# Kernel tuning notes

Measured on AMD Instinct MI355X. Metric: run time of the kernel, lower is better.

Reference implementation:

```python
import jax, jax.numpy as jnp
import numpy as np

NUM_USERS = 50000
NUM_ITEMS = 100000
N = NUM_USERS + NUM_ITEMS
D = 64
K = 3
E = 1000000


def setup_inputs() -> dict:
    key = jax.random.key(0)
    k1, k2, k3, k4 = jax.random.split(key, 4)
    users_emb = jax.random.normal(k1, (NUM_USERS, D), dtype=jnp.float32)
    items_emb = jax.random.normal(k2, (NUM_ITEMS, D), dtype=jnp.float32)
    src = jax.random.randint(k3, (E,), 0, N, dtype=jnp.int32)
    dst = jax.random.randint(k4, (E,), 0, N, dtype=jnp.int32)
    return {"users_emb": users_emb, "items_emb": items_emb, "src": src, "dst": dst}


def reference(users_emb, items_emb, src, dst):
    all_emb = jnp.concatenate([users_emb, items_emb], axis=0)  # [N, D]
    # out_degrees: number of outgoing edges per node, clamped to >= 1
    deg = jax.ops.segment_sum(jnp.ones((E,), dtype=jnp.float32), src, num_segments=N)
    normed_deg = jnp.power(jnp.clip(deg, 1.0, None), -0.5)[:, None]  # [N, 1]

    def conv(emb):
        h = emb * normed_deg                                  # D^{-1/2} * x
        agg = jax.ops.segment_sum(h[src], dst, num_segments=N)  # copy_u + sum
        return agg * normed_deg                               # * D^{-1/2}

    acc = all_emb
    emb = all_emb
    for _ in range(K):
        emb = conv(emb)
        acc = acc + emb
    final = acc / (K + 1)  # mean over layer embeddings
    return final[:NUM_USERS], final[NUM_USERS:]
```

## Files before the change

kernel.cpp:

```cpp
#include <hip/hip_runtime.h>

#define NUSERS 50000
#define NITEMS 100000
#define NNODES 150000
#define DIM 64
#define BSTRIDE 32

static __device__ __forceinline__ unsigned short f2bf(float f) {
    unsigned u = __float_as_uint(f);
    return (unsigned short)((u + 0x7fffu + ((u >> 16) & 1u)) >> 16);
}
static __device__ __forceinline__ unsigned pack2(float lo, float hi) {
    return (unsigned)f2bf(lo) | ((unsigned)f2bf(hi) << 16);
}
static __device__ __forceinline__ void acc8(float* sum, uint4 u) {
    sum[0] += __uint_as_float(u.x << 16);
    sum[1] += __uint_as_float(u.x & 0xffff0000u);
    sum[2] += __uint_as_float(u.y << 16);
    sum[3] += __uint_as_float(u.y & 0xffff0000u);
    sum[4] += __uint_as_float(u.z << 16);
    sum[5] += __uint_as_float(u.z & 0xffff0000u);
    sum[6] += __uint_as_float(u.w << 16);
    sum[7] += __uint_as_float(u.w & 0xffff0000u);
}

__global__ void hist_place_kernel(const int* __restrict__ src,
                                  const int* __restrict__ dst,
                                  int* __restrict__ outdeg,
                                  int* __restrict__ indeg,
                                  int* __restrict__ csr, int E) {
    int e = blockIdx.x * blockDim.x + threadIdx.x;
    if (e >= E) return;
    int s = src[e];
    int d = dst[e];
    atomicAdd(&outdeg[s], 1);
    int r = atomicAdd(&indeg[d], 1);
    if (r < BSTRIDE) csr[d * BSTRIDE + r] = s;
}

__global__ void prescale_kernel(const float4* __restrict__ users4,
                                const float4* __restrict__ items4,
                                const int* __restrict__ outdeg,
                                uint4* __restrict__ s0) {
    int t = blockIdx.x * blockDim.x + threadIdx.x;
    int v = t >> 3;
    int l = t & 7;
    if (v >= NNODES) return;
    float ns = rsqrtf(fmaxf((float)outdeg[v], 1.0f));
    const float4* rowp = (v < NUSERS) ? users4 + (size_t)v * 16
                                      : items4 + (size_t)(v - NUSERS) * 16;
    float4 a = rowp[l * 2];
    float4 b = rowp[l * 2 + 1];
    uint4 p;
    p.x = pack2(a.x * ns, a.y * ns);
    p.y = pack2(a.z * ns, a.w * ns);
    p.z = pack2(b.x * ns, b.y * ns);
    p.w = pack2(b.z * ns, b.w * ns);
    s0[(size_t)v * 8 + l] = p;
}

__global__ void gather_mid_kernel(const int4* __restrict__ csr4,
                                  const int* __restrict__ indeg,
                                  const int* __restrict__ outdeg,
                                  const uint4* __restrict__ cur,
                                  uint4* __restrict__ nxt) {
    int t = blockIdx.x * blockDim.x + threadIdx.x;
    int v = t >> 3;
    int l = t & 7;
    if (v >= NNODES) return;
    int cnt = min(indeg[v], BSTRIDE);
    const int4* bucket = csr4 + (size_t)v * (BSTRIDE / 4);
    float sum[8] = {0.f, 0.f, 0.f, 0.f, 0.f, 0.f, 0.f, 0.f};
    int groups = (cnt + 3) >> 2;
    for (int kk = 0; kk < groups; ++kk) {
        int4 c = bucket[kk];
        int base = kk * 4;
        if (base + 0 < cnt) acc8(sum, cur[(size_t)c.x * 8 + l]);
        if (base + 1 < cnt) acc8(sum, cur[(size_t)c.y * 8 + l]);
        if (base + 2 < cnt) acc8(sum, cur[(size_t)c.z * 8 + l]);
        if (base + 3 < cnt) acc8(sum, cur[(size_t)c.w * 8 + l]);
    }
    float inv_d = 1.0f / fmaxf((float)outdeg[v], 1.0f);
    uint4 p;
    p.x = pack2(sum[0] * inv_d, sum[1] * inv_d);
    p.y = pack2(sum[2] * inv_d, sum[3] * inv_d);
    p.z = pack2(sum[4] * inv_d, sum[5] * inv_d);
    p.w = pack2(sum[6] * inv_d, sum[7] * inv_d);
    nxt[(size_t)v * 8 + l] = p;
}

__global__ void gather_last_kernel(const int4* __restrict__ csr4,
                                   const int* __restrict__ indeg,
                                   const int* __restrict__ outdeg,
                                   const uint4* __restrict__ s2,
                                   const uint4* __restrict__ s1,
                                   const float4* __restrict__ users4,
                                   const float4* __restrict__ items4,
                                   float4* __restrict__ out4) {
    int t = blockIdx.x * blockDim.x + threadIdx.x;
    int v = t >> 3;
    int l = t & 7;
    if (v >= NNODES) return;
    int cnt = min(indeg[v], BSTRIDE);
    const int4* bucket = csr4 + (size_t)v * (BSTRIDE / 4);
    float sum[8] = {0.f, 0.f, 0.f, 0.f, 0.f, 0.f, 0.f, 0.f};
    int groups = (cnt + 3) >> 2;
    for (int kk = 0; kk < groups; ++kk) {
        int4 c = bucket[kk];
        int base = kk * 4;
        if (base + 0 < cnt) acc8(sum, s2[(size_t)c.x * 8 + l]);
        if (base + 1 < cnt) acc8(sum, s2[(size_t)c.y * 8 + l]);
        if (base + 2 < cnt) acc8(sum, s2[(size_t)c.z * 8 + l]);
        if (base + 3 < cnt) acc8(sum, s2[(size_t)c.w * 8 + l]);
    }
    float d  = fmaxf((float)outdeg[v], 1.0f);
    float ns = rsqrtf(d);
    float sq = d * ns;
    size_t o = (size_t)v * 8 + l;
    const float4* rowp = (v < NUSERS) ? users4 + (size_t)v * 16
                                      : items4 + (size_t)(v - NUSERS) * 16;
    float4 oa = rowp[l * 2];
    float4 ob = rowp[l * 2 + 1];
    uint4 u1 = s1[o];
    uint4 u2 = s2[o];
    float a12[8];
    a12[0] = __uint_as_float(u1.x << 16)        + __uint_as_float(u2.x << 16);
    a12[1] = __uint_as_float(u1.x & 0xffff0000u) + __uint_as_float(u2.x & 0xffff0000u);
    a12[2] = __uint_as_float(u1.y << 16)        + __uint_as_float(u2.y << 16);
    a12[3] = __uint_as_float(u1.y & 0xffff0000u) + __uint_as_float(u2.y & 0xffff0000u);
    a12[4] = __uint_as_float(u1.z << 16)        + __uint_as_float(u2.z << 16);
    a12[5] = __uint_as_float(u1.z & 0xffff0000u) + __uint_as_float(u2.z & 0xffff0000u);
    a12[6] = __uint_as_float(u1.w << 16)        + __uint_as_float(u2.w << 16);
    a12[7] = __uint_as_float(u1.w & 0xffff0000u) + __uint_as_float(u2.w & 0xffff0000u);
    float4 r0, r1;
    r0.x = (oa.x + a12[0] * sq + sum[0] * ns) * 0.25f;
    r0.y = (oa.y + a12[1] * sq + sum[1] * ns) * 0.25f;
    r0.z = (oa.z + a12[2] * sq + sum[2] * ns) * 0.25f;
    r0.w = (oa.w + a12[3] * sq + sum[3] * ns) * 0.25f;
    r1.x = (ob.x + a12[4] * sq + sum[4] * ns) * 0.25f;
    r1.y = (ob.y + a12[5] * sq + sum[5] * ns) * 0.25f;
    r1.z = (ob.z + a12[6] * sq + sum[6] * ns) * 0.25f;
    r1.w = (ob.w + a12[7] * sq + sum[7] * ns) * 0.25f;
    out4[(size_t)v * 16 + l * 2]     = r0;
    out4[(size_t)v * 16 + l * 2 + 1] = r1;
}

extern "C" void kernel_launch(void* const* d_in, const int* in_sizes, int n_in,
                              void* d_out, int out_size, void* d_ws, size_t ws_size,
                              hipStream_t stream) {
    const int* src = (const int*)d_in[2];
    const int* dst = (const int*)d_in[3];
    const int  E   = in_sizes[2];
    const float4* users4 = (const float4*)d_in[0];
    const float4* items4 = (const float4*)d_in[1];
    float4* out4 = (float4*)d_out;

    char* w = (char*)d_ws;
    int*   outdeg = (int*)w;   w += sizeof(int) * NNODES;
    int*   indeg  = (int*)w;   w += sizeof(int) * NNODES;
    int*   csr    = (int*)w;   w += sizeof(int) * (size_t)NNODES * BSTRIDE;
    uint4* s0     = (uint4*)w; w += sizeof(unsigned short) * (size_t)NNODES * DIM;
    uint4* s1     = (uint4*)w; w += sizeof(unsigned short) * (size_t)NNODES * DIM;
    uint4* s2     = (uint4*)w;

    const int BLK  = 256;
    const int gedg = (E + BLK - 1) / BLK;
    const int ggat = (NNODES * 8 + BLK - 1) / BLK;

    hipMemsetAsync(outdeg, 0, sizeof(int) * NNODES * 2, stream);
    hist_place_kernel<<<gedg, BLK, 0, stream>>>(src, dst, outdeg, indeg, csr, E);
    prescale_kernel<<<ggat, BLK, 0, stream>>>(users4, items4, outdeg, s0);

    gather_mid_kernel<<<ggat, BLK, 0, stream>>>((const int4*)csr, indeg, outdeg, s0, s1);
    gather_mid_kernel<<<ggat, BLK, 0, stream>>>((const int4*)csr, indeg, outdeg, s1, s2);
    gather_last_kernel<<<ggat, BLK, 0, stream>>>((const int4*)csr, indeg, outdeg,
                                                 s2, s1, users4, items4, out4);
}
```

Baseline: 212.5 us.

## Split degree histogram and co-schedule CSR placement with prescale; unroll first gather group

The out-degree histogram now runs as its own kernel. CSR bucket placement is merged with the bf16 prescale into one launch, with blocks split by index, so the atomic-heavy placement overlaps the bandwidth-bound prescale. The gather kernels load the first two index groups up front and unroll the first eight neighbours, which exposes more independent loads. In exchange, src is read twice and one extra kernel launch is added.

```diff
diff --git a/kernel.cpp b/kernel.cpp
--- a/kernel.cpp
+++ b/kernel.cpp
@@ -24,39 +24,45 @@
     sum[7] += __uint_as_float(u.w & 0xffff0000u);
 }
 
-__global__ void hist_place_kernel(const int* __restrict__ src,
-                                  const int* __restrict__ dst,
-                                  int* __restrict__ outdeg,
-                                  int* __restrict__ indeg,
-                                  int* __restrict__ csr, int E) {
+__global__ void outdeg_kernel(const int* __restrict__ src,
+                              int* __restrict__ outdeg, int E) {
     int e = blockIdx.x * blockDim.x + threadIdx.x;
-    if (e >= E) return;
-    int s = src[e];
-    int d = dst[e];
-    atomicAdd(&outdeg[s], 1);
-    int r = atomicAdd(&indeg[d], 1);
-    if (r < BSTRIDE) csr[d * BSTRIDE + r] = s;
-}
-
-__global__ void prescale_kernel(const float4* __restrict__ users4,
-                                const float4* __restrict__ items4,
-                                const int* __restrict__ outdeg,
-                                uint4* __restrict__ s0) {
-    int t = blockIdx.x * blockDim.x + threadIdx.x;
-    int v = t >> 3;
-    int l = t & 7;
-    if (v >= NNODES) return;
-    float ns = rsqrtf(fmaxf((float)outdeg[v], 1.0f));
-    const float4* rowp = (v < NUSERS) ? users4 + (size_t)v * 16
-                                      : items4 + (size_t)(v - NUSERS) * 16;
-    float4 a = rowp[l * 2];
-    float4 b = rowp[l * 2 + 1];
-    uint4 p;
-    p.x = pack2(a.x * ns, a.y * ns);
-    p.y = pack2(a.z * ns, a.w * ns);
-    p.z = pack2(b.x * ns, b.y * ns);
-    p.w = pack2(b.z * ns, b.w * ns);
-    s0[(size_t)v * 8 + l] = p;
+    if (e < E) atomicAdd(&outdeg[src[e]], 1);
+}
+
+__global__ void place_prescale_kernel(const int* __restrict__ src,
+                                      const int* __restrict__ dst,
+                                      const float4* __restrict__ users4,
+                                      const float4* __restrict__ items4,
+                                      const int* __restrict__ outdeg,
+                                      int* __restrict__ indeg,
+                                      int* __restrict__ csr,
+                                      uint4* __restrict__ s0,
+                                      int E, int GP) {
+    if ((int)blockIdx.x < GP) {
+        int e = blockIdx.x * 256 + threadIdx.x;
+        if (e >= E) return;
+        int s = src[e];
+        int d = dst[e];
+        int r = atomicAdd(&indeg[d], 1);
+        if (r < BSTRIDE) csr[d * BSTRIDE + r] = s;
+    } else {
+        int t = ((int)blockIdx.x - GP) * 256 + threadIdx.x;
+        int v = t >> 3;
+        int l = t & 7;
+        if (v >= NNODES) return;
+        float ns = rsqrtf(fmaxf((float)outdeg[v], 1.0f));
+        const float4* rowp = (v < NUSERS) ? users4 + (size_t)v * 16
+                                          : items4 + (size_t)(v - NUSERS) * 16;
+        float4 a = rowp[l * 2];
+        float4 b = rowp[l * 2 + 1];
+        uint4 p;
+        p.x = pack2(a.x * ns, a.y * ns);
+        p.y = pack2(a.z * ns, a.w * ns);
+        p.z = pack2(b.x * ns, b.y * ns);
+        p.w = pack2(b.z * ns, b.w * ns);
+        s0[(size_t)v * 8 + l] = p;
+    }
 }
 
 __global__ void gather_mid_kernel(const int4* __restrict__ csr4,
@@ -71,14 +77,26 @@
     int cnt = min(indeg[v], BSTRIDE);
     const int4* bucket = csr4 + (size_t)v * (BSTRIDE / 4);
     float sum[8] = {0.f, 0.f, 0.f, 0.f, 0.f, 0.f, 0.f, 0.f};
-    int groups = (cnt + 3) >> 2;
-    for (int kk = 0; kk < groups; ++kk) {
-        int4 c = bucket[kk];
-        int base = kk * 4;
-        if (base + 0 < cnt) acc8(sum, cur[(size_t)c.x * 8 + l]);
-        if (base + 1 < cnt) acc8(sum, cur[(size_t)c.y * 8 + l]);
-        if (base + 2 < cnt) acc8(sum, cur[(size_t)c.z * 8 + l]);
-        if (base + 3 < cnt) acc8(sum, cur[(size_t)c.w * 8 + l]);
+    int4 c0 = bucket[0];
+    int4 c1 = bucket[1];
+    if (0 < cnt) acc8(sum, cur[(size_t)c0.x * 8 + l]);
+    if (1 < cnt) acc8(sum, cur[(size_t)c0.y * 8 + l]);
+    if (2 < cnt) acc8(sum, cur[(size_t)c0.z * 8 + l]);
+    if (3 < cnt) acc8(sum, cur[(size_t)c0.w * 8 + l]);
+    if (4 < cnt) acc8(sum, cur[(size_t)c1.x * 8 + l]);
+    if (5 < cnt) acc8(sum, cur[(size_t)c1.y * 8 + l]);
+    if (6 < cnt) acc8(sum, cur[(size_t)c1.z * 8 + l]);
+    if (7 < cnt) acc8(sum, cur[(size_t)c1.w * 8 + l]);
+    if (cnt > 8) {
+        int groups = (cnt + 3) >> 2;
+        for (int kk = 2; kk < groups; ++kk) {
+            int4 c = bucket[kk];
+            int base = kk * 4;
+            if (base + 0 < cnt) acc8(sum, cur[(size_t)c.x * 8 + l]);
+            if (base + 1 < cnt) acc8(sum, cur[(size_t)c.y * 8 + l]);
+            if (base + 2 < cnt) acc8(sum, cur[(size_t)c.z * 8 + l]);
+            if (base + 3 < cnt) acc8(sum, cur[(size_t)c.w * 8 + l]);
+        }
     }
     float inv_d = 1.0f / fmaxf((float)outdeg[v], 1.0f);
     uint4 p;
@@ -104,14 +122,26 @@
     int cnt = min(indeg[v], BSTRIDE);
     const int4* bucket = csr4 + (size_t)v * (BSTRIDE / 4);
     float sum[8] = {0.f, 0.f, 0.f, 0.f, 0.f, 0.f, 0.f, 0.f};
-    int groups = (cnt + 3) >> 2;
-    for (int kk = 0; kk < groups; ++kk) {
-        int4 c = bucket[kk];
-        int base = kk * 4;
-        if (base + 0 < cnt) acc8(sum, s2[(size_t)c.x * 8 + l]);
-        if (base + 1 < cnt) acc8(sum, s2[(size_t)c.y * 8 + l]);
-        if (base + 2 < cnt) acc8(sum, s2[(size_t)c.z * 8 + l]);
-        if (base + 3 < cnt) acc8(sum, s2[(size_t)c.w * 8 + l]);
+    int4 c0 = bucket[0];
+    int4 c1 = bucket[1];
+    if (0 < cnt) acc8(sum, s2[(size_t)c0.x * 8 + l]);
+    if (1 < cnt) acc8(sum, s2[(size_t)c0.y * 8 + l]);
+    if (2 < cnt) acc8(sum, s2[(size_t)c0.z * 8 + l]);
+    if (3 < cnt) acc8(sum, s2[(size_t)c0.w * 8 + l]);
+    if (4 < cnt) acc8(sum, s2[(size_t)c1.x * 8 + l]);
+    if (5 < cnt) acc8(sum, s2[(size_t)c1.y * 8 + l]);
+    if (6 < cnt) acc8(sum, s2[(size_t)c1.z * 8 + l]);
+    if (7 < cnt) acc8(sum, s2[(size_t)c1.w * 8 + l]);
+    if (cnt > 8) {
+        int groups = (cnt + 3) >> 2;
+        for (int kk = 2; kk < groups; ++kk) {
+            int4 c = bucket[kk];
+            int base = kk * 4;
+            if (base + 0 < cnt) acc8(sum, s2[(size_t)c.x * 8 + l]);
+            if (base + 1 < cnt) acc8(sum, s2[(size_t)c.y * 8 + l]);
+            if (base + 2 < cnt) acc8(sum, s2[(size_t)c.z * 8 + l]);
+            if (base + 3 < cnt) acc8(sum, s2[(size_t)c.w * 8 + l]);
+        }
     }
     float d  = fmaxf((float)outdeg[v], 1.0f);
     float ns = rsqrtf(d);
@@ -124,13 +154,13 @@
     uint4 u1 = s1[o];
     uint4 u2 = s2[o];
     float a12[8];
-    a12[0] = __uint_as_float(u1.x << 16)        + __uint_as_float(u2.x << 16);
+    a12[0] = __uint_as_float(u1.x << 16)         + __uint_as_float(u2.x << 16);
     a12[1] = __uint_as_float(u1.x & 0xffff0000u) + __uint_as_float(u2.x & 0xffff0000u);
-    a12[2] = __uint_as_float(u1.y << 16)        + __uint_as_float(u2.y << 16);
+    a12[2] = __uint_as_float(u1.y << 16)         + __uint_as_float(u2.y << 16);
     a12[3] = __uint_as_float(u1.y & 0xffff0000u) + __uint_as_float(u2.y & 0xffff0000u);
-    a12[4] = __uint_as_float(u1.z << 16)        + __uint_as_float(u2.z << 16);
+    a12[4] = __uint_as_float(u1.z << 16)         + __uint_as_float(u2.z << 16);
     a12[5] = __uint_as_float(u1.z & 0xffff0000u) + __uint_as_float(u2.z & 0xffff0000u);
-    a12[6] = __uint_as_float(u1.w << 16)        + __uint_as_float(u2.w << 16);
+    a12[6] = __uint_as_float(u1.w << 16)         + __uint_as_float(u2.w << 16);
     a12[7] = __uint_as_float(u1.w & 0xffff0000u) + __uint_as_float(u2.w & 0xffff0000u);
     float4 r0, r1;
     r0.x = (oa.x + a12[0] * sq + sum[0] * ns) * 0.25f;
@@ -165,11 +195,14 @@
 
     const int BLK  = 256;
     const int gedg = (E + BLK - 1) / BLK;
+    const int gpre = (NNODES * 8 + BLK - 1) / BLK;
     const int ggat = (NNODES * 8 + BLK - 1) / BLK;
 
     hipMemsetAsync(outdeg, 0, sizeof(int) * NNODES * 2, stream);
-    hist_place_kernel<<<gedg, BLK, 0, stream>>>(src, dst, outdeg, indeg, csr, E);
-    prescale_kernel<<<ggat, BLK, 0, stream>>>(users4, items4, outdeg, s0);
+    outdeg_kernel<<<gedg, BLK, 0, stream>>>(src, outdeg, E);
+    place_prescale_kernel<<<gedg + gpre, BLK, 0, stream>>>(src, dst, users4, items4,
+                                                           outdeg, indeg, csr, s0,
+                                                           E, gedg);
 
     gather_mid_kernel<<<ggat, BLK, 0, stream>>>((const int4*)csr, indeg, outdeg, s0, s1);
     gather_mid_kernel<<<ggat, BLK, 0, stream>>>((const int4*)csr, indeg, outdeg, s1, s2);
```

Result: no change. 214.0 us (+0.7%).
